# Kernel optimization log

Hardware: AMD Instinct MI355X
Metric: run time of the kernel (lower is better)

Reference implementation:

```python
import jax, jax.numpy as jnp
import numpy as np

NUM_STEPS = 8
ADD_IDENTITY = True
EPS = 1e-12
STANDARDIZE = True


def setup_inputs() -> dict:
    key = jax.random.key(0)
    N = 4096
    E = 65536  # avg degree 16
    edge_index = jax.random.randint(key, (2, E), 0, N, dtype=jnp.int64 if jax.config.jax_enable_x64 else jnp.int32)
    edge_weight = jnp.ones((E,), dtype=jnp.float32)
    return {"edge_index": edge_index, "edge_weight": edge_weight, "num_nodes": N}


def reference(edge_index, edge_weight, num_nodes):
    # A[i,j] = sum of edge_weight over edges (row=i, col=j); scipy sums duplicates,
    # and segment_sum does the same.
    row, col = edge_index[0], edge_index[1]
    # deg_j = column sums of A (A.sum(axis=0))
    deg = jax.ops.segment_sum(edge_weight, col, num_segments=num_nodes)
    deg = jnp.maximum(deg, EPS)
    # M = A @ D^{-1}:  M[row, col] = w / deg[col]
    w = edge_weight / deg[col]  # [E]

    # Carry dense propagator P = M^t, extract diagonals for t = 1..NUM_STEPS.
    P0 = jnp.eye(num_nodes, dtype=jnp.float32)  # [N, N]

    def step(P, _):
        # P_new[i, :] = sum_{edges (i=row, j=col)} w_e * P[j, :]
        P = jax.ops.segment_sum(w[:, None] * P[col], row, num_segments=num_nodes)
        return P, jnp.diagonal(P)

    _, diags = jax.lax.scan(step, P0, None, length=NUM_STEPS)  # [T, N]

    X = diags.T  # [N, T]
    if ADD_IDENTITY:
        X = jnp.concatenate([jnp.ones((num_nodes, 1), dtype=jnp.float32), X], axis=1)
    if STANDARDIZE:
        mean = X.mean(axis=0, keepdims=True)
        std = jnp.maximum(X.std(axis=0, keepdims=True), 1e-6)  # ddof=0 == unbiased=False
        X = (X - mean) / std
    return X
```

## Files before the change

### kernel.cpp

```cpp
#include <hip/hip_runtime.h>

#define NN 4096
#define TSTEPS 8
#define EPSW 1e-12f
#define SLABW 512
#define NSLAB 8
#define LSLAB 9
#define SLAB_ELEMS ((size_t)NN * SLABW)

typedef unsigned int uint32;
typedef uint32 uint4v __attribute__((ext_vector_type(4)));

__device__ __forceinline__ uint32 bf16rn(float f) {
  uint32 b = __float_as_uint(f);
  return (b + 0x7FFFu + ((b >> 16) & 1u)) >> 16;
}
__device__ __forceinline__ float bf2f(ushort u) {
  return __uint_as_float(((uint32)u) << 16);
}

__global__ __launch_bounds__(256) void deg_counts_kernel(
    const int* __restrict__ rows, const int* __restrict__ cols,
    const float* __restrict__ ew, float* __restrict__ deg,
    int* __restrict__ counts, int E) {
  int e = blockIdx.x * 256 + threadIdx.x;
  if (e >= E) return;
  atomicAdd(deg + cols[e], ew[e]);
  atomicAdd(counts + rows[e], 1);
}

__global__ __launch_bounds__(1024) void scan_kernel(const int* __restrict__ counts,
                                                    int* __restrict__ row_ptr) {
  __shared__ int sm[1024];
  int tid = threadIdx.x;
  int b = tid * 4;
  int c0 = counts[b], c1 = counts[b + 1], c2 = counts[b + 2], c3 = counts[b + 3];
  sm[tid] = c0 + c1 + c2 + c3;
  __syncthreads();
  for (int off = 1; off < 1024; off <<= 1) {
    int v = (tid >= off) ? sm[tid - off] : 0;
    __syncthreads();
    sm[tid] += v;
    __syncthreads();
  }
  int excl = (tid == 0) ? 0 : sm[tid - 1];
  row_ptr[b]     = excl;
  row_ptr[b + 1] = excl + c0;
  row_ptr[b + 2] = excl + c0 + c1;
  row_ptr[b + 3] = excl + c0 + c1 + c2;
  if (tid == 1023) row_ptr[NN] = sm[1023];
}

__global__ __launch_bounds__(256) void csr_scatter_kernel(
    const int* __restrict__ rows, const int* __restrict__ cols,
    const float* __restrict__ ew, const float* __restrict__ deg,
    const int* __restrict__ row_ptr, int* __restrict__ fill,
    int* __restrict__ col_s, float* __restrict__ w_s,
    float* __restrict__ diags, int E) {
  int e = blockIdx.x * 256 + threadIdx.x;
  if (e >= E) return;
  int r = rows[e], c = cols[e];
  float w = ew[e] / fmaxf(deg[c], EPSW);
  int pos = row_ptr[r] + atomicAdd(fill + r, 1);
  col_s[pos] = c;
  w_s[pos] = w;
  if (r == c) atomicAdd(diags + r, w);
}

__global__ __launch_bounds__(64) void m2_csr_kernel(
    const int* __restrict__ row_ptr, const int* __restrict__ col_s,
    const float* __restrict__ w_s, ushort* __restrict__ dst,
    float* __restrict__ diags) {
  int i = blockIdx.x;
  int tid = threadIdx.x;
  __shared__ float acc[NN];
  __shared__ int sc[64];
  __shared__ float sw[64];
#pragma unroll
  for (int k = 0; k < NN / 64; ++k) acc[k * 64 + tid] = 0.f;
  int e0 = row_ptr[i], e1 = row_ptr[i + 1];
  __syncthreads();
  for (int base = e0; base < e1; base += 64) {
    int cnt = min(64, e1 - base);
    if (tid < cnt) {
      sc[tid] = col_s[base + tid];
      sw[tid] = w_s[base + tid];
    }
    __syncthreads();
    for (int e = 0; e < cnt; ++e) {
      int j = sc[e];
      float we = sw[e];
      int f0 = row_ptr[j], f1 = row_ptr[j + 1];
      for (int f = f0 + tid; f < f1; f += 64)
        atomicAdd(acc + col_s[f], we * w_s[f]);
    }
    __syncthreads();
  }
  if (tid == 0) diags[NN + i] = acc[i];
#pragma unroll
  for (int k = 0; k < NN / 64; ++k) {
    int c = k * 64 + tid;
    ushort h = (ushort)bf16rn(acc[c]);
    size_t idx = ((size_t)(c >> LSLAB)) * SLAB_ELEMS + (size_t)i * SLABW + (c & (SLABW - 1));
    __builtin_nontemporal_store(h, dst + idx);
  }
}

__global__ __launch_bounds__(64) void spmm_kernel(
    const ushort* __restrict__ src, ushort* __restrict__ dst,
    const int* __restrict__ row_ptr, const int* __restrict__ col_s,
    const float* __restrict__ w_s, float* __restrict__ diags, int tIdx) {
  int bid = blockIdx.x;
  int slab = bid & (NSLAB - 1);
  int i = bid >> 3;
  int tid = threadIdx.x;
  int e0 = row_ptr[i], e1 = row_ptr[i + 1];
  __shared__ int sc[64];
  __shared__ float sw[64];
  float acc[8];
#pragma unroll
  for (int q = 0; q < 8; ++q) acc[q] = 0.f;
  const ushort* sbase = src + (size_t)slab * SLAB_ELEMS + tid * 8;

  for (int base = e0; base < e1; base += 64) {
    int cnt = min(64, e1 - base);
    if (tid < cnt) {
      sc[tid] = col_s[base + tid];
      sw[tid] = w_s[base + tid];
    }
    __syncthreads();
    int k = 0;
    for (; k + 4 <= cnt; k += 4) {
      uint4v u0 = *(const uint4v*)(sbase + ((size_t)sc[k]     << LSLAB));
      uint4v u1 = *(const uint4v*)(sbase + ((size_t)sc[k + 1] << LSLAB));
      uint4v u2 = *(const uint4v*)(sbase + ((size_t)sc[k + 2] << LSLAB));
      uint4v u3 = *(const uint4v*)(sbase + ((size_t)sc[k + 3] << LSLAB));
      float w0 = sw[k], w1 = sw[k + 1], w2 = sw[k + 2], w3 = sw[k + 3];
#pragma unroll
      for (int q = 0; q < 4; ++q) {
        acc[2 * q]     += w0 * __uint_as_float(u0[q] << 16);
        acc[2 * q + 1] += w0 * __uint_as_float(u0[q] & 0xFFFF0000u);
      }
#pragma unroll
      for (int q = 0; q < 4; ++q) {
        acc[2 * q]     += w1 * __uint_as_float(u1[q] << 16);
        acc[2 * q + 1] += w1 * __uint_as_float(u1[q] & 0xFFFF0000u);
      }
#pragma unroll
      for (int q = 0; q < 4; ++q) {
        acc[2 * q]     += w2 * __uint_as_float(u2[q] << 16);
        acc[2 * q + 1] += w2 * __uint_as_float(u2[q] & 0xFFFF0000u);
      }
#pragma unroll
      for (int q = 0; q < 4; ++q) {
        acc[2 * q]     += w3 * __uint_as_float(u3[q] << 16);
        acc[2 * q + 1] += w3 * __uint_as_float(u3[q] & 0xFFFF0000u);
      }
    }
    for (; k < cnt; ++k) {
      uint4v u = *(const uint4v*)(sbase + ((size_t)sc[k] << LSLAB));
      float w = sw[k];
#pragma unroll
      for (int q = 0; q < 4; ++q) {
        acc[2 * q]     += w * __uint_as_float(u[q] << 16);
        acc[2 * q + 1] += w * __uint_as_float(u[q] & 0xFFFF0000u);
      }
    }
    __syncthreads();
  }

  uint4v o;
#pragma unroll
  for (int q = 0; q < 4; ++q)
    o[q] = bf16rn(acc[2 * q]) | (bf16rn(acc[2 * q + 1]) << 16);
  __builtin_nontemporal_store(
      o, (uint4v*)(dst + (size_t)slab * SLAB_ELEMS + (size_t)i * SLABW + tid * 8));

  if ((i >> LSLAB) == slab) {
    int lc = i & (SLABW - 1);
    if ((lc >> 3) == tid) {
      int m = lc & 7;
      float v = acc[0];
      v = (m == 1) ? acc[1] : v;
      v = (m == 2) ? acc[2] : v;
      v = (m == 3) ? acc[3] : v;
      v = (m == 4) ? acc[4] : v;
      v = (m == 5) ? acc[5] : v;
      v = (m == 6) ? acc[6] : v;
      v = (m == 7) ? acc[7] : v;
      diags[tIdx * NN + i] = v;
    }
  }
}

__device__ __forceinline__ size_t slab_addr(int row, int col) {
  return ((size_t)(col >> LSLAB)) * SLAB_ELEMS + (size_t)row * SLABW + (col & (SLABW - 1));
}
__device__ __forceinline__ float elem8(uint4v lo, uint4v hi, int c) {
  uint32 u = (c < 8) ? lo[(c & 7) >> 1] : hi[(c & 7) >> 1];
  return __uint_as_float((c & 1) ? (u & 0xFFFF0000u) : (u << 16));
}

__global__ __launch_bounds__(256) void trace_kernel(
    const ushort* __restrict__ M2, const ushort* __restrict__ M3,
    const ushort* __restrict__ M4, float* __restrict__ diags) {
  int bid = blockIdx.x;
  int bi = bid >> 3, jc = bid & 7;
  int tid = threadIdx.x;
  __shared__ ushort b3[64 * 64], b4[64 * 64];
  __shared__ float red[4][4][64];
  int lr = tid >> 2, lc0 = (tid & 3) * 16;
  int r = tid & 63, jq = tid >> 6;
  float s5 = 0.f, s6 = 0.f, s7 = 0.f, s8 = 0.f;

  for (int it = 0; it < 8; ++it) {
    int bj = jc * 8 + it;
    {
      int gj = bj * 64 + lr;
      int gc = bi * 64 + lc0;
      size_t base = slab_addr(gj, gc);
      uint4v v3a = *(const uint4v*)(M3 + base);
      uint4v v3b = *(const uint4v*)(M3 + base + 8);
      uint4v v4a = *(const uint4v*)(M4 + base);
      uint4v v4b = *(const uint4v*)(M4 + base + 8);
      int cb0 = (lc0 >> 3) ^ (lr & 7);
      int cb1 = ((lc0 >> 3) + 1) ^ (lr & 7);
      *(uint4v*)(b3 + lr * 64 + cb0 * 8) = v3a;
      *(uint4v*)(b3 + lr * 64 + cb1 * 8) = v3b;
      *(uint4v*)(b4 + lr * 64 + cb0 * 8) = v4a;
      *(uint4v*)(b4 + lr * 64 + cb1 * 8) = v4b;
    }
    __syncthreads();
    int gi = bi * 64 + r;
    int gc0 = bj * 64 + jq * 16;
    size_t abase = slab_addr(gi, gc0);
    uint4v a2a = *(const uint4v*)(M2 + abase);
    uint4v a2b = *(const uint4v*)(M2 + abase + 8);
    uint4v a3a = *(const uint4v*)(M3 + abase);
    uint4v a3b = *(const uint4v*)(M3 + abase + 8);
    uint4v a4a = *(const uint4v*)(M4 + abase);
    uint4v a4b = *(const uint4v*)(M4 + abase + 8);
#pragma unroll
    for (int c = 0; c < 16; ++c) {
      int jj = jq * 16 + c;
      int idx = jj * 64 + ((((r >> 3) ^ (jj & 7)) << 3) | (r & 7));
      float bv3 = bf2f(b3[idx]);
      float bv4 = bf2f(b4[idx]);
      float av2 = elem8(a2a, a2b, c);
      float av3 = elem8(a3a, a3b, c);
      float av4 = elem8(a4a, a4b, c);
      s5 += av2 * bv3;
      s6 += av3 * bv3;
      s7 += av3 * bv4;
      s8 += av4 * bv4;
    }
    __syncthreads();
  }
  red[0][jq][r] = s5;
  red[1][jq][r] = s6;
  red[2][jq][r] = s7;
  red[3][jq][r] = s8;
  __syncthreads();
  if (tid < 64) {
    int gi = bi * 64 + tid;
#pragma unroll
    for (int v = 0; v < 4; ++v) {
      float s = red[v][0][tid] + red[v][1][tid] + red[v][2][tid] + red[v][3][tid];
      atomicAdd(diags + (4 + v) * NN + gi, s);
    }
  }
}

__global__ __launch_bounds__(256) void finalize_kernel(const float* __restrict__ diags,
                                                       float* __restrict__ out) {
  int k = blockIdx.x;
  int tid = threadIdx.x;
  float vals[16];
  float sum = 0.f, sq = 0.f;
#pragma unroll
  for (int j = 0; j < 16; ++j) {
    int i = j * 256 + tid;
    float v = (k == 0) ? 1.0f : diags[(k - 1) * NN + i];
    vals[j] = v;
    sum += v;
    sq += v * v;
  }
#pragma unroll
  for (int off = 32; off; off >>= 1) {
    sum += __shfl_down(sum, off);
    sq += __shfl_down(sq, off);
  }
  __shared__ float s0[4], s1[4];
  __shared__ float smean, sinv;
  int wid = tid >> 6, lane = tid & 63;
  if (lane == 0) { s0[wid] = sum; s1[wid] = sq; }
  __syncthreads();
  if (tid == 0) {
    float S = s0[0] + s0[1] + s0[2] + s0[3];
    float Q = s1[0] + s1[1] + s1[2] + s1[3];
    float mean = S / (float)NN;
    float var = Q / (float)NN - mean * mean;
    var = fmaxf(var, 0.f);
    float sd = fmaxf(sqrtf(var), 1e-6f);
    smean = mean;
    sinv = 1.f / sd;
  }
  __syncthreads();
#pragma unroll
  for (int j = 0; j < 16; ++j) {
    int i = j * 256 + tid;
    out[i * (TSTEPS + 1) + k] = (vals[j] - smean) * sinv;
  }
}

extern "C" void kernel_launch(void* const* d_in, const int* in_sizes, int n_in,
                              void* d_out, int out_size, void* d_ws, size_t ws_size,
                              hipStream_t stream) {
  const int* ei = (const int*)d_in[0];
  const float* ew = (const float*)d_in[1];
  int E = in_sizes[1];
  const int* rows = ei;
  const int* cols = ei + E;

  char* ws = (char*)d_ws;
  size_t off = 0;
  auto alloc = [&](size_t bytes) {
    void* p = ws + off;
    off = (off + bytes + 255) & ~(size_t)255;
    return p;
  };
  float* deg     = (float*)alloc(NN * 4);
  int*   counts  = (int*)alloc(NN * 4);
  int*   fill    = (int*)alloc(NN * 4);
  int*   row_ptr = (int*)alloc((NN + 1) * 4);
  int*   col_s   = (int*)alloc((size_t)E * 4);
  float* w_s     = (float*)alloc((size_t)E * 4);
  float* diags   = (float*)alloc((size_t)TSTEPS * NN * 4);
  ushort* bufA   = (ushort*)alloc((size_t)NN * NN * 2);
  ushort* bufB   = (ushort*)alloc((size_t)NN * NN * 2);
  ushort* bufC   = (ushort*)alloc((size_t)NN * NN * 2);

  hipMemsetAsync(deg, 0, NN * 4, stream);
  hipMemsetAsync(counts, 0, NN * 4, stream);
  hipMemsetAsync(fill, 0, NN * 4, stream);
  hipMemsetAsync(diags, 0, (size_t)TSTEPS * NN * 4, stream);

  int eb = (E + 255) / 256;
  deg_counts_kernel<<<eb, 256, 0, stream>>>(rows, cols, ew, deg, counts, E);
  scan_kernel<<<1, 1024, 0, stream>>>(counts, row_ptr);
  csr_scatter_kernel<<<eb, 256, 0, stream>>>(rows, cols, ew, deg, row_ptr, fill,
                                             col_s, w_s, diags, E);

  m2_csr_kernel<<<NN, 64, 0, stream>>>(row_ptr, col_s, w_s, bufA, diags);
  spmm_kernel<<<NN * NSLAB, 64, 0, stream>>>(bufA, bufB, row_ptr, col_s, w_s, diags, 2);
  spmm_kernel<<<NN * NSLAB, 64, 0, stream>>>(bufB, bufC, row_ptr, col_s, w_s, diags, 3);
  trace_kernel<<<512, 256, 0, stream>>>(bufA, bufB, bufC, diags);

  finalize_kernel<<<TSTEPS + 1, 256, 0, stream>>>(diags, (float*)d_out);
}
```

Baseline: 146.7 us.

## Broadcast edges via readlane, swizzle LDS accumulator, pack spmm rows into 256-thread blocks

Replaces the shared-memory staging of edge columns and weights, along with its barriers, with per-lane registers broadcast through readlane in both the M² and SpMM kernels. The M² kernel now uses an XOR-swizzled LDS accumulator so the output can be read with vectorized float4 loads and written as 16-byte non-temporal stores. SpMM now packs four rows per 256-thread block, one wave per row, cutting the block count by four. Four separate memsets become one by placing the zeroed buffers next to each other. The trade-off is that SpMM loses its manual 4-way load unrolling, which may reduce memory-level parallelism.

```diff
diff --git a/kernel.cpp b/kernel.cpp
--- a/kernel.cpp
+++ b/kernel.cpp
@@ -17,6 +17,13 @@
 }
 __device__ __forceinline__ float bf2f(ushort u) {
   return __uint_as_float(((uint32)u) << 16);
+}
+__device__ __forceinline__ float rdlanef(float v, int k) {
+  return __uint_as_float(__builtin_amdgcn_readlane(__float_as_uint(v), k));
+}
+__device__ __forceinline__ int sphys(int c) {
+  int blk = c >> 3;
+  return ((blk ^ ((blk >> 3) & 7)) << 3) | (c & 7);
 }
 
 __global__ __launch_bounds__(256) void deg_counts_kernel(
@@ -74,99 +81,72 @@
   int i = blockIdx.x;
   int tid = threadIdx.x;
   __shared__ float acc[NN];
-  __shared__ int sc[64];
-  __shared__ float sw[64];
-#pragma unroll
-  for (int k = 0; k < NN / 64; ++k) acc[k * 64 + tid] = 0.f;
+  float4 z4 = make_float4(0.f, 0.f, 0.f, 0.f);
+#pragma unroll
+  for (int k = 0; k < 16; ++k) *(float4*)(acc + k * 256 + tid * 4) = z4;
   int e0 = row_ptr[i], e1 = row_ptr[i + 1];
   __syncthreads();
   for (int base = e0; base < e1; base += 64) {
     int cnt = min(64, e1 - base);
-    if (tid < cnt) {
-      sc[tid] = col_s[base + tid];
-      sw[tid] = w_s[base + tid];
-    }
-    __syncthreads();
+    int myc = 0;
+    float myw = 0.f;
+    if (tid < cnt) { myc = col_s[base + tid]; myw = w_s[base + tid]; }
     for (int e = 0; e < cnt; ++e) {
-      int j = sc[e];
-      float we = sw[e];
+      int j = __builtin_amdgcn_readlane(myc, e);
+      float we = rdlanef(myw, e);
       int f0 = row_ptr[j], f1 = row_ptr[j + 1];
       for (int f = f0 + tid; f < f1; f += 64)
-        atomicAdd(acc + col_s[f], we * w_s[f]);
-    }
-    __syncthreads();
-  }
-  if (tid == 0) diags[NN + i] = acc[i];
-#pragma unroll
-  for (int k = 0; k < NN / 64; ++k) {
-    int c = k * 64 + tid;
-    ushort h = (ushort)bf16rn(acc[c]);
-    size_t idx = ((size_t)(c >> LSLAB)) * SLAB_ELEMS + (size_t)i * SLABW + (c & (SLABW - 1));
-    __builtin_nontemporal_store(h, dst + idx);
-  }
-}
-
-__global__ __launch_bounds__(64) void spmm_kernel(
+        atomicAdd(acc + sphys(col_s[f]), we * w_s[f]);
+    }
+  }
+  __syncthreads();
+  if (tid == 0) diags[NN + i] = acc[sphys(i)];
+#pragma unroll
+  for (int p = 0; p < 8; ++p) {
+    int c = p * SLABW + tid * 8;
+    int ph = sphys(c);
+    float4 lo = *(const float4*)(acc + ph);
+    float4 hi = *(const float4*)(acc + ph + 4);
+    uint4v o;
+    o.x = bf16rn(lo.x) | (bf16rn(lo.y) << 16);
+    o.y = bf16rn(lo.z) | (bf16rn(lo.w) << 16);
+    o.z = bf16rn(hi.x) | (bf16rn(hi.y) << 16);
+    o.w = bf16rn(hi.z) | (bf16rn(hi.w) << 16);
+    __builtin_nontemporal_store(
+        o, (uint4v*)(dst + (size_t)p * SLAB_ELEMS + (size_t)i * SLABW + tid * 8));
+  }
+}
+
+__global__ __launch_bounds__(256) void spmm_kernel(
     const ushort* __restrict__ src, ushort* __restrict__ dst,
     const int* __restrict__ row_ptr, const int* __restrict__ col_s,
     const float* __restrict__ w_s, float* __restrict__ diags, int tIdx) {
-  int bid = blockIdx.x;
-  int slab = bid & (NSLAB - 1);
-  int i = bid >> 3;
-  int tid = threadIdx.x;
+  int b = blockIdx.x;
+  int slab = b & (NSLAB - 1);
+  int wv = threadIdx.x >> 6;
+  int lane = threadIdx.x & 63;
+  int i = ((b >> 3) << 2) | wv;
   int e0 = row_ptr[i], e1 = row_ptr[i + 1];
-  __shared__ int sc[64];
-  __shared__ float sw[64];
   float acc[8];
 #pragma unroll
   for (int q = 0; q < 8; ++q) acc[q] = 0.f;
-  const ushort* sbase = src + (size_t)slab * SLAB_ELEMS + tid * 8;
+  const ushort* sbase = src + (size_t)slab * SLAB_ELEMS + lane * 8;
 
   for (int base = e0; base < e1; base += 64) {
     int cnt = min(64, e1 - base);
-    if (tid < cnt) {
-      sc[tid] = col_s[base + tid];
-      sw[tid] = w_s[base + tid];
-    }
-    __syncthreads();
-    int k = 0;
-    for (; k + 4 <= cnt; k += 4) {
-      uint4v u0 = *(const uint4v*)(sbase + ((size_t)sc[k]     << LSLAB));
-      uint4v u1 = *(const uint4v*)(sbase + ((size_t)sc[k + 1] << LSLAB));
-      uint4v u2 = *(const uint4v*)(sbase + ((size_t)sc[k + 2] << LSLAB));
-      uint4v u3 = *(const uint4v*)(sbase + ((size_t)sc[k + 3] << LSLAB));
-      float w0 = sw[k], w1 = sw[k + 1], w2 = sw[k + 2], w3 = sw[k + 3];
-#pragma unroll
-      for (int q = 0; q < 4; ++q) {
-        acc[2 * q]     += w0 * __uint_as_float(u0[q] << 16);
-        acc[2 * q + 1] += w0 * __uint_as_float(u0[q] & 0xFFFF0000u);
-      }
-#pragma unroll
-      for (int q = 0; q < 4; ++q) {
-        acc[2 * q]     += w1 * __uint_as_float(u1[q] << 16);
-        acc[2 * q + 1] += w1 * __uint_as_float(u1[q] & 0xFFFF0000u);
-      }
-#pragma unroll
-      for (int q = 0; q < 4; ++q) {
-        acc[2 * q]     += w2 * __uint_as_float(u2[q] << 16);
-        acc[2 * q + 1] += w2 * __uint_as_float(u2[q] & 0xFFFF0000u);
-      }
-#pragma unroll
-      for (int q = 0; q < 4; ++q) {
-        acc[2 * q]     += w3 * __uint_as_float(u3[q] << 16);
-        acc[2 * q + 1] += w3 * __uint_as_float(u3[q] & 0xFFFF0000u);
-      }
-    }
-    for (; k < cnt; ++k) {
-      uint4v u = *(const uint4v*)(sbase + ((size_t)sc[k] << LSLAB));
-      float w = sw[k];
+    int myc = 0;
+    float myw = 0.f;
+    if (lane < cnt) { myc = col_s[base + lane]; myw = w_s[base + lane]; }
+    for (int k = 0; k < cnt; ++k) {
+      int c = __builtin_amdgcn_readlane(myc, k);
+      float w = rdlanef(myw, k);
+      uint4v u = *(const uint4v*)(sbase + ((size_t)c << LSLAB));
 #pragma unroll
       for (int q = 0; q < 4; ++q) {
         acc[2 * q]     += w * __uint_as_float(u[q] << 16);
         acc[2 * q + 1] += w * __uint_as_float(u[q] & 0xFFFF0000u);
       }
     }
-    __syncthreads();
   }
 
   uint4v o;
@@ -174,11 +154,11 @@
   for (int q = 0; q < 4; ++q)
     o[q] = bf16rn(acc[2 * q]) | (bf16rn(acc[2 * q + 1]) << 16);
   __builtin_nontemporal_store(
-      o, (uint4v*)(dst + (size_t)slab * SLAB_ELEMS + (size_t)i * SLABW + tid * 8));
+      o, (uint4v*)(dst + (size_t)slab * SLAB_ELEMS + (size_t)i * SLABW + lane * 8));
 
   if ((i >> LSLAB) == slab) {
     int lc = i & (SLABW - 1);
-    if ((lc >> 3) == tid) {
+    if ((lc >> 3) == lane) {
       int m = lc & 7;
       float v = acc[0];
       v = (m == 1) ? acc[1] : v;
@@ -332,18 +312,16 @@
   float* deg     = (float*)alloc(NN * 4);
   int*   counts  = (int*)alloc(NN * 4);
   int*   fill    = (int*)alloc(NN * 4);
+  float* diags   = (float*)alloc((size_t)TSTEPS * NN * 4);
+  size_t zbytes  = off;
   int*   row_ptr = (int*)alloc((NN + 1) * 4);
   int*   col_s   = (int*)alloc((size_t)E * 4);
   float* w_s     = (float*)alloc((size_t)E * 4);
-  float* diags   = (float*)alloc((size_t)TSTEPS * NN * 4);
   ushort* bufA   = (ushort*)alloc((size_t)NN * NN * 2);
   ushort* bufB   = (ushort*)alloc((size_t)NN * NN * 2);
   ushort* bufC   = (ushort*)alloc((size_t)NN * NN * 2);
 
-  hipMemsetAsync(deg, 0, NN * 4, stream);
-  hipMemsetAsync(counts, 0, NN * 4, stream);
-  hipMemsetAsync(fill, 0, NN * 4, stream);
-  hipMemsetAsync(diags, 0, (size_t)TSTEPS * NN * 4, stream);
+  hipMemsetAsync(deg, 0, zbytes, stream);
 
   int eb = (E + 255) / 256;
   deg_counts_kernel<<<eb, 256, 0, stream>>>(rows, cols, ew, deg, counts, E);
@@ -352,8 +330,8 @@
                                              col_s, w_s, diags, E);
 
   m2_csr_kernel<<<NN, 64, 0, stream>>>(row_ptr, col_s, w_s, bufA, diags);
-  spmm_kernel<<<NN * NSLAB, 64, 0, stream>>>(bufA, bufB, row_ptr, col_s, w_s, diags, 2);
-  spmm_kernel<<<NN * NSLAB, 64, 0, stream>>>(bufB, bufC, row_ptr, col_s, w_s, diags, 3);
+  spmm_kernel<<<(NN / 4) * NSLAB, 256, 0, stream>>>(bufA, bufB, row_ptr, col_s, w_s, diags, 2);
+  spmm_kernel<<<(NN / 4) * NSLAB, 256, 0, stream>>>(bufB, bufC, row_ptr, col_s, w_s, diags, 3);
   trace_kernel<<<512, 256, 0, stream>>>(bufA, bufB, bufC, diags);
 
   finalize_kernel<<<TSTEPS + 1, 256, 0, stream>>>(diags, (float*)d_out);
```

Result: slower. 159.5 us (+8.7%).
